# Optimization experiments

Measured on AMD Instinct MI355X. Metric: run time of the kernel, lower is better.

The kernel has to match this reference:

```python
import jax, jax.numpy as jnp
import numpy as np

B, N, E, D, H, L = 1, 50000, 800000, 128, 8, 3
HD = D // H
VOCAB = 7000
OUT = 10


def _ln(x, g, b, eps=1e-5):
    m = x.mean(-1, keepdims=True)
    v = ((x - m) ** 2).mean(-1, keepdims=True)
    return (x - m) * jax.lax.rsqrt(v + eps) * g + b


def setup_inputs() -> dict:
    key = jax.random.key(0)
    ks = jax.random.split(key, 40)
    std = 0.02 / np.sqrt(L)

    def w(k, shape):
        return (jax.random.normal(k, shape, jnp.float32) * std)

    inp = {
        "x_idx": jax.random.randint(ks[0], (B, N, 1), 0, VOCAB),
        "edge_index": jax.random.randint(ks[1], (2, E), 0, B * N),
        "emb": jax.random.normal(ks[2], (VOCAB, D), jnp.float32) * 0.02,
        # per-layer params stacked on leading L axis; linears stored [in, out]
        "Wq": w(ks[3], (L, D, D)), "bq": jnp.zeros((L, D), jnp.float32),
        "Wk": w(ks[4], (L, D, D)), "bk": jnp.zeros((L, D), jnp.float32),
        "Wv": w(ks[5], (L, D, D)), "bv": jnp.zeros((L, D), jnp.float32),
        "Wo": w(ks[6], (L, D, D)), "bo": jnp.zeros((L, D), jnp.float32),
        "g1": jnp.ones((L, D), jnp.float32), "be1": jnp.zeros((L, D), jnp.float32),
        "Wf1": w(ks[7], (L, D, 2 * D)), "bf1": jnp.zeros((L, 2 * D), jnp.float32),
        "Wf2": w(ks[8], (L, 2 * D, D)), "bf2": jnp.zeros((L, D), jnp.float32),
        "g2": jnp.ones((L, D), jnp.float32), "be2": jnp.zeros((L, D), jnp.float32),
        # MLPReadout: D -> D/2 -> D/4 -> OUT
        "mW0": w(ks[9], (D, D // 2)), "mb0": jnp.zeros((D // 2,), jnp.float32),
        "mW1": w(ks[10], (D // 2, D // 4)), "mb1": jnp.zeros((D // 4,), jnp.float32),
        "mW2": w(ks[11], (D // 4, OUT)), "mb2": jnp.zeros((OUT,), jnp.float32),
    }
    return inp


def reference(x_idx, edge_index, emb, Wq, bq, Wk, bk, Wv, bv, Wo, bo,
              g1, be1, Wf1, bf1, Wf2, bf2, g2, be2,
              mW0, mb0, mW1, mb1, mW2, mb2):
    # node embedding: sum over feature-index axis -> [B, N, D]
    x = emb[x_idx].sum(axis=-2)
    e0, e1 = edge_index[0], edge_index[1]
    scale = jnp.sqrt(jnp.float32(HD))

    for l in range(L):
        h = x
        hf = h.reshape(B * N, D)
        q = (hf @ Wq[l] + bq[l]).reshape(B * N, H, HD)
        k = (hf @ Wk[l] + bk[l]).reshape(B * N, H, HD)
        v = (hf @ Wv[l] + bv[l]).reshape(B * N, H, HD)
        # edge-indexed gather-mul-exp  [E, H, 1]
        score = jnp.clip(jnp.sum(k[e0] * q[e1], axis=-1, keepdims=True) / scale,
                         -5.0, 5.0)
        score = jnp.exp(score)
        msg = v[e0] * score                                    # [E, H, HD]
        wV = jax.ops.segment_sum(msg, e1, num_segments=B * N)  # [B*N, H, HD]
        Z = jax.ops.segment_sum(score, e1, num_segments=B * N) # [B*N, H, 1]
        attn = (wV / (Z + 1e-6)).reshape(B, N, D)
        y = attn @ Wo[l] + bo[l]
        x = _ln(h + y, g1[l], be1[l])
        # note: FFN input is y (attention output), per the original code
        y2 = jnp.maximum(y @ Wf1[l] + bf1[l], 0.0) @ Wf2[l] + bf2[l]
        x = _ln(x + y2, g2[l], be2[l])

    out = x.mean(axis=1)  # [B, D]
    out = jnp.maximum(out @ mW0 + mb0, 0.0)
    out = jnp.maximum(out @ mW1 + mb1, 0.0)
    return out @ mW2 + mb2  # [B, OUT]
```

## Files before the change

kernel.cpp:

```cpp
#include <hip/hip_runtime.h>
#include <hip/hip_bf16.h>

#define N_NODES 50000
#define N_EDGES 800000
#define DIM 128
#define NLAYERS 3

typedef short bf16x8 __attribute__((ext_vector_type(8)));
typedef float floatx4 __attribute__((ext_vector_type(4)));
typedef float floatx2 __attribute__((ext_vector_type(2)));

__device__ __forceinline__ unsigned short f2bf(float f) {
  unsigned int u = __builtin_bit_cast(unsigned int, f);
  return (unsigned short)((u + 0x7FFFu + ((u >> 16) & 1u)) >> 16);
}
__device__ __forceinline__ float bf2f(unsigned short h) {
  return __builtin_bit_cast(float, (unsigned int)h << 16);
}

__global__ __launch_bounds__(256) void embed_kernel(
    const int* __restrict__ idx, const float* __restrict__ emb,
    unsigned short* __restrict__ xb)
{
  int gid = blockIdx.x * 256 + threadIdx.x;
  int n = gid >> 5;
  int c = (gid & 31) << 2;
  if (n >= N_NODES) return;
  int e = idx[n];
  float4 val = *(const float4*)(emb + (size_t)e * DIM + c);
  ushort4 pk;
  pk.x = f2bf(val.x); pk.y = f2bf(val.y); pk.z = f2bf(val.z); pk.w = f2bf(val.w);
  *(ushort4*)(xb + (size_t)n * DIM + c) = pk;
}

__global__ __launch_bounds__(256) void hist_kernel(
    const int* __restrict__ e1, int* __restrict__ counts,
    int* __restrict__ rank)
{
  int i = blockIdx.x * 256 + threadIdx.x;
  if (i < N_EDGES) rank[i] = atomicAdd(&counts[e1[i]], 1);
}

__global__ __launch_bounds__(256) void scan_local(
    const int* __restrict__ counts, int* __restrict__ offsets,
    int* __restrict__ bsums)
{
  __shared__ int buf[256];
  int t = threadIdx.x;
  int i = blockIdx.x * 256 + t;
  int v = (i < N_NODES) ? counts[i] : 0;
  buf[t] = v;
  __syncthreads();
  int s = v;
#pragma unroll
  for (int off = 1; off < 256; off <<= 1) {
    int t2 = (t >= off) ? buf[t - off] : 0;
    __syncthreads();
    s += t2;
    buf[t] = s;
    __syncthreads();
  }
  if (i < N_NODES) offsets[i] = s - v;
  if (t == 255) bsums[blockIdx.x] = s;
}

__global__ void scan_bsums(int* __restrict__ bsums, int nblk)
{
  __shared__ int buf[256];
  int t = threadIdx.x;
  int v = (t < nblk) ? bsums[t] : 0;
  buf[t] = v;
  __syncthreads();
  int s = v;
#pragma unroll
  for (int off = 1; off < 256; off <<= 1) {
    int t2 = (t >= off) ? buf[t - off] : 0;
    __syncthreads();
    s += t2;
    buf[t] = s;
    __syncthreads();
  }
  if (t < nblk) bsums[t] = s - v;
}

__global__ __launch_bounds__(256) void scan_add(
    int* __restrict__ offsets, const int* __restrict__ bsums)
{
  int i = blockIdx.x * 256 + threadIdx.x;
  if (i < N_NODES) offsets[i] += bsums[blockIdx.x];
  if (i == 0) offsets[N_NODES] = N_EDGES;
}

__global__ __launch_bounds__(256) void scatter_kernel(
    const int* __restrict__ e0, const int* __restrict__ e1,
    const int* __restrict__ offsets, const int* __restrict__ rank,
    int* __restrict__ csr)
{
  int i = blockIdx.x * 256 + threadIdx.x;
  if (i >= N_EDGES) return;
  csr[offsets[e1[i]] + rank[i]] = e0[i];
}

__global__ __launch_bounds__(256) void prep_all(
    const float* __restrict__ Wq, const float* __restrict__ Wk,
    const float* __restrict__ Wv, const float* __restrict__ Wo,
    const float* __restrict__ Wf1, const float* __restrict__ Wf2,
    unsigned short* __restrict__ wqkv, unsigned short* __restrict__ wo,
    unsigned short* __restrict__ wf1, unsigned short* __restrict__ wf2)
{
  int g = blockIdx.x * 256 + threadIdx.x;
  if (g < 18432) {
    int srcId = g / 6144; int rem = g - srcId * 6144;
    const float* W = (srcId == 0) ? Wq : (srcId == 1) ? Wk : Wv;
    int l = rem / 2048; int r2 = rem & 2047; int kq = r2 >> 7; int n = r2 & 127;
    const float* Wl = W + (size_t)l * 128 * 128;
    unsigned short* base = wqkv + (size_t)l * 128 * 384 + (size_t)(kq * 384 + srcId * 128 + n) * 8;
#pragma unroll
    for (int j = 0; j < 8; j++)
      base[j] = f2bf(Wl[(size_t)(kq * 8 + j) * 128 + n]);
    return;
  }
  g -= 18432;
  if (g < 6144) {
    int l = g / 2048; int r2 = g & 2047; int kq = r2 >> 7; int n = r2 & 127;
    const float* Wl = Wo + (size_t)l * 128 * 128;
    unsigned short* base = wo + (size_t)l * 128 * 128 + (size_t)(kq * 128 + n) * 8;
#pragma unroll
    for (int j = 0; j < 8; j++)
      base[j] = f2bf(Wl[(size_t)(kq * 8 + j) * 128 + n]);
    return;
  }
  g -= 6144;
  if (g < 12288) {
    int l = g / 4096; int r2 = g & 4095; int kq = r2 >> 8; int n = r2 & 255;
    const float* Wl = Wf1 + (size_t)l * 128 * 256;
    unsigned short* base = wf1 + (size_t)l * 128 * 256 + (size_t)(kq * 256 + n) * 8;
#pragma unroll
    for (int j = 0; j < 8; j++)
      base[j] = f2bf(Wl[(size_t)(kq * 8 + j) * 256 + n]);
    return;
  }
  g -= 12288;
  if (g < 12288) {
    int l = g / 4096; int r2 = g & 4095; int kq = r2 >> 7; int n = r2 & 127;
    const float* Wl = Wf2 + (size_t)l * 256 * 128;
    unsigned short* base = wf2 + (size_t)l * 256 * 128 + (size_t)(kq * 128 + n) * 8;
#pragma unroll
    for (int j = 0; j < 8; j++)
      base[j] = f2bf(Wl[(size_t)(kq * 8 + j) * 128 + n]);
  }
}

#define LSTR 136

__global__ __launch_bounds__(256) void qkv0_kernel(
    const unsigned short* __restrict__ xb,
    const unsigned short* __restrict__ wqkv,
    const float* __restrict__ bq, const float* __restrict__ bk,
    const float* __restrict__ bv,
    unsigned short* __restrict__ qkv, int nrows)
{
  __shared__ unsigned short XR[64 * LSTR];
  int tid = threadIdx.x;
  int wave = tid >> 6, lane = tid & 63;
  int quad = lane >> 4, l16 = lane & 15;
  int rbase = blockIdx.x * 64;
  int wrow = wave * 16;
  int rowg = min(rbase + wrow + l16, nrows - 1);
  int lrow_v = (wrow + l16) * LSTR + quad * 8;
  bool wr = (rbase + wrow + l16 < nrows);

  bf16x8 avQ[4];
  {
    const unsigned short* arow = xb + (size_t)rowg * 128 + quad * 8;
#pragma unroll
    for (int kb = 0; kb < 4; kb++)
      avQ[kb] = *(const bf16x8*)(arow + kb * 32);
  }
#pragma unroll
  for (int c = 0; c < 3; c++) {
    floatx4 accQ[8];
#pragma unroll
    for (int ct = 0; ct < 8; ct++) accQ[ct] = (floatx4)(0.f);
#pragma unroll
    for (int kb = 0; kb < 4; kb++) {
      int kq = kb * 4 + quad;
      bf16x8 bh[8];
#pragma unroll
      for (int ct = 0; ct < 8; ct++)
        bh[ct] = *(const bf16x8*)&wqkv[(size_t)(kq * 384 + c * 128 + ct * 16 + l16) * 8];
#pragma unroll
      for (int ct = 0; ct < 8; ct++)
        accQ[ct] = __builtin_amdgcn_mfma_f32_16x16x32_bf16(avQ[kb], bh[ct], accQ[ct], 0, 0, 0);
    }
    const float* bias = (c == 0) ? bq : (c == 1) ? bk : bv;
#pragma unroll
    for (int ct = 0; ct < 8; ct++) {
      float bvv = bias[ct * 16 + l16];
#pragma unroll
      for (int i = 0; i < 4; i++)
        XR[(wrow + quad * 4 + i) * LSTR + ct * 16 + l16] = f2bf(accQ[ct][i] + bvv);
    }
    if (wr) {
      if (c == 0) {
#pragma unroll
        for (int kb = 0; kb < 4; kb++)
          *(bf16x8*)&qkv[(size_t)(rbase + wrow + l16) * 256 + kb * 32 + quad * 8] =
              *(bf16x8*)&XR[lrow_v + kb * 32];
      } else {
#pragma unroll
        for (int kb = 0; kb < 4; kb++) {
          bf16x8 w = *(bf16x8*)&XR[lrow_v + kb * 32];
          int p0 = __builtin_amdgcn_cvt_pk_fp8_f32(
              bf2f((unsigned short)w[0]) * 8.f, bf2f((unsigned short)w[1]) * 8.f, 0, false);
          int p1 = __builtin_amdgcn_cvt_pk_fp8_f32(
              bf2f((unsigned short)w[2]) * 8.f, bf2f((unsigned short)w[3]) * 8.f, 0, false);
          int p2 = __builtin_amdgcn_cvt_pk_fp8_f32(
              bf2f((unsigned short)w[4]) * 8.f, bf2f((unsigned short)w[5]) * 8.f, 0, false);
          int p3 = __builtin_amdgcn_cvt_pk_fp8_f32(
              bf2f((unsigned short)w[6]) * 8.f, bf2f((unsigned short)w[7]) * 8.f, 0, false);
          int2 st;
          st.x = (p0 & 0xffff) | (p1 << 16);
          st.y = (p2 & 0xffff) | (p3 << 16);
          *(int2*)&qkv[(size_t)(rbase + wrow + l16) * 256 + 128 + (c - 1) * 64 +
                       kb * 16 + quad * 4] = st;
        }
      }
    }
  }
}

template<bool LAST>
__global__ __launch_bounds__(256) void chainM_kernel(
    const unsigned short* __restrict__ a,
    unsigned short* __restrict__ xb,
    unsigned short* __restrict__ qkv,
    const unsigned short* __restrict__ wo, const float* __restrict__ bo,
    const float* __restrict__ g1, const float* __restrict__ be1,
    const unsigned short* __restrict__ wf1, const float* __restrict__ bf1,
    const unsigned short* __restrict__ wf2, const float* __restrict__ bf2,
    const float* __restrict__ g2, const float* __restrict__ be2,
    const unsigned short* __restrict__ wqkv,
    const float* __restrict__ bq, const float* __restrict__ bk,
    const float* __restrict__ bv, int nrows)
{
  __shared__ unsigned short Y[64 * LSTR];
  __shared__ unsigned short F[64 * LSTR];
  int tid = threadIdx.x;
  int wave = tid >> 6, lane = tid & 63;
  int quad = lane >> 4, l16 = lane & 15;
  int rbase = blockIdx.x * 64;
  int wrow = wave * 16;
  int rowg = min(rbase + wrow + l16, nrows - 1);
  int lrow_v = (wrow + l16) * LSTR + quad * 8;
  bool wr = (rbase + wrow + l16 < nrows);

#pragma unroll
  for (int kb = 0; kb < 4; kb++)
    *(bf16x8*)&F[lrow_v + kb * 32] =
        *(const bf16x8*)&xb[(size_t)rowg * 128 + kb * 32 + quad * 8];

  floatx4 accO[8];
#pragma unroll
  for (int cc = 0; cc < 8; cc++) accO[cc] = (floatx4)(0.f);
  {
    const unsigned short* arow = a + (size_t)rowg * 128 + quad * 8;
#pragma unroll
    for (int kb = 0; kb < 4; kb++) {
      bf16x8 av = *(const bf16x8*)(arow + kb * 32);
      int kq = kb * 4 + quad;
      bf16x8 bh[8];
#pragma unroll
      for (int cc = 0; cc < 8; cc++)
        bh[cc] = *(const bf16x8*)&wo[(size_t)(kq * 128 + cc * 16 + l16) * 8];
#pragma unroll
      for (int cc = 0; cc < 8; cc++)
        accO[cc] = __builtin_amdgcn_mfma_f32_16x16x32_bf16(av, bh[cc], accO[cc], 0, 0, 0);
    }
  }

  float x1v[8][4];
  {
    float biasO[8], g1v[8], b1v[8];
#pragma unroll
    for (int cc = 0; cc < 8; cc++) {
      int col = cc * 16 + l16;
      biasO[cc] = bo[col]; g1v[cc] = g1[col]; b1v[cc] = be1[col];
    }
#pragma unroll
    for (int i = 0; i < 4; i++) {
      int lrow = wrow + quad * 4 + i;
      float t[8]; float s = 0.f;
#pragma unroll
      for (int cc = 0; cc < 8; cc++) {
        float yv = accO[cc][i] + biasO[cc];
        Y[lrow * LSTR + cc * 16 + l16] = f2bf(yv);
        t[cc] = yv + bf2f(F[lrow * LSTR + cc * 16 + l16]);
        s += t[cc];
      }
      s += __shfl_xor(s, 1); s += __shfl_xor(s, 2);
      s += __shfl_xor(s, 4); s += __shfl_xor(s, 8);
      float mean = s * (1.f / 128.f);
      float vv = 0.f;
#pragma unroll
      for (int cc = 0; cc < 8; cc++) { float d = t[cc] - mean; vv += d * d; }
      vv += __shfl_xor(vv, 1); vv += __shfl_xor(vv, 2);
      vv += __shfl_xor(vv, 4); vv += __shfl_xor(vv, 8);
      float inv = rsqrtf(vv * (1.f / 128.f) + 1e-5f);
#pragma unroll
      for (int cc = 0; cc < 8; cc++)
        x1v[cc][i] = bf2f(f2bf((t[cc] - mean) * inv * g1v[cc] + b1v[cc]));
    }
  }

  bf16x8 avY[4];
#pragma unroll
  for (int kb = 0; kb < 4; kb++)
    avY[kb] = *(bf16x8*)&Y[lrow_v + kb * 32];
  floatx4 acc2[8];
#pragma unroll
  for (int cc = 0; cc < 8; cc++) acc2[cc] = (floatx4)(0.f);
#pragma unroll
  for (int h = 0; h < 2; h++) {
    floatx4 accF[8];
#pragma unroll
    for (int cc = 0; cc < 8; cc++) accF[cc] = (floatx4)(0.f);
#pragma unroll
    for (int kb = 0; kb < 4; kb++) {
      int kq = kb * 4 + quad;
      bf16x8 bh[8];
#pragma unroll
      for (int cc = 0; cc < 8; cc++)
        bh[cc] = *(const bf16x8*)&wf1[(size_t)(kq * 256 + h * 128 + cc * 16 + l16) * 8];
#pragma unroll
      for (int cc = 0; cc < 8; cc++)
        accF[cc] = __builtin_amdgcn_mfma_f32_16x16x32_bf16(avY[kb], bh[cc], accF[cc], 0, 0, 0);
    }
#pragma unroll
    for (int i = 0; i < 4; i++) {
      int lrow = wrow + quad * 4 + i;
#pragma unroll
      for (int cc = 0; cc < 8; cc++)
        F[lrow * LSTR + cc * 16 + l16] =
            f2bf(fmaxf(accF[cc][i] + bf1[h * 128 + cc * 16 + l16], 0.f));
    }
#pragma unroll
    for (int kb = 0; kb < 4; kb++) {
      bf16x8 avF = *(bf16x8*)&F[lrow_v + kb * 32];
      int kq = h * 16 + kb * 4 + quad;
      bf16x8 bh[8];
#pragma unroll
      for (int cc = 0; cc < 8; cc++)
        bh[cc] = *(const bf16x8*)&wf2[(size_t)(kq * 128 + cc * 16 + l16) * 8];
#pragma unroll
      for (int cc = 0; cc < 8; cc++)
        acc2[cc] = __builtin_amdgcn_mfma_f32_16x16x32_bf16(avF, bh[cc], acc2[cc], 0, 0, 0);
    }
  }

  {
    float bias2[8], g2v[8], b2v[8];
#pragma unroll
    for (int cc = 0; cc < 8; cc++) {
      int col = cc * 16 + l16;
      bias2[cc] = bf2[col]; g2v[cc] = g2[col]; b2v[cc] = be2[col];
    }
#pragma unroll
    for (int i = 0; i < 4; i++) {
      int lrow = wrow + quad * 4 + i;
      float t[8]; float s = 0.f;
#pragma unroll
      for (int cc = 0; cc < 8; cc++) {
        t[cc] = acc2[cc][i] + bias2[cc] + x1v[cc][i];
        s += t[cc];
      }
      s += __shfl_xor(s, 1); s += __shfl_xor(s, 2);
      s += __shfl_xor(s, 4); s += __shfl_xor(s, 8);
      float mean = s * (1.f / 128.f);
      float vv = 0.f;
#pragma unroll
      for (int cc = 0; cc < 8; cc++) { float d = t[cc] - mean; vv += d * d; }
      vv += __shfl_xor(vv, 1); vv += __shfl_xor(vv, 2);
      vv += __shfl_xor(vv, 4); vv += __shfl_xor(vv, 8);
      float inv = rsqrtf(vv * (1.f / 128.f) + 1e-5f);
#pragma unroll
      for (int cc = 0; cc < 8; cc++)
        Y[lrow * LSTR + cc * 16 + l16] =
            f2bf((t[cc] - mean) * inv * g2v[cc] + b2v[cc]);
    }
  }
  if (wr) {
#pragma unroll
    for (int kb = 0; kb < 4; kb++)
      *(bf16x8*)&xb[(size_t)(rbase + wrow + l16) * 128 + kb * 32 + quad * 8] =
          *(bf16x8*)&Y[lrow_v + kb * 32];
  }

  if (!LAST) {
    bf16x8 avQ[4];
#pragma unroll
    for (int kb = 0; kb < 4; kb++)
      avQ[kb] = *(bf16x8*)&Y[lrow_v + kb * 32];
#pragma unroll
    for (int c = 0; c < 3; c++) {
      floatx4 accQ[8];
#pragma unroll
      for (int ct = 0; ct < 8; ct++) accQ[ct] = (floatx4)(0.f);
#pragma unroll
      for (int kb = 0; kb < 4; kb++) {
        int kq = kb * 4 + quad;
        bf16x8 bh[8];
#pragma unroll
        for (int ct = 0; ct < 8; ct++)
          bh[ct] = *(const bf16x8*)&wqkv[(size_t)(kq * 384 + c * 128 + ct * 16 + l16) * 8];
#pragma unroll
        for (int ct = 0; ct < 8; ct++)
          accQ[ct] = __builtin_amdgcn_mfma_f32_16x16x32_bf16(avQ[kb], bh[ct], accQ[ct], 0, 0, 0);
      }
      const float* bias = (c == 0) ? bq : (c == 1) ? bk : bv;
#pragma unroll
      for (int ct = 0; ct < 8; ct++) {
        float bvv = bias[ct * 16 + l16];
#pragma unroll
        for (int i = 0; i < 4; i++)
          F[(wrow + quad * 4 + i) * LSTR + ct * 16 + l16] = f2bf(accQ[ct][i] + bvv);
      }
      if (wr) {
        if (c == 0) {
#pragma unroll
          for (int kb = 0; kb < 4; kb++)
            *(bf16x8*)&qkv[(size_t)(rbase + wrow + l16) * 256 + kb * 32 + quad * 8] =
                *(bf16x8*)&F[lrow_v + kb * 32];
        } else {
#pragma unroll
          for (int kb = 0; kb < 4; kb++) {
            bf16x8 w = *(bf16x8*)&F[lrow_v + kb * 32];
            int p0 = __builtin_amdgcn_cvt_pk_fp8_f32(
                bf2f((unsigned short)w[0]) * 8.f, bf2f((unsigned short)w[1]) * 8.f, 0, false);
            int p1 = __builtin_amdgcn_cvt_pk_fp8_f32(
                bf2f((unsigned short)w[2]) * 8.f, bf2f((unsigned short)w[3]) * 8.f, 0, false);
            int p2 = __builtin_amdgcn_cvt_pk_fp8_f32(
                bf2f((unsigned short)w[4]) * 8.f, bf2f((unsigned short)w[5]) * 8.f, 0, false);
            int p3 = __builtin_amdgcn_cvt_pk_fp8_f32(
                bf2f((unsigned short)w[6]) * 8.f, bf2f((unsigned short)w[7]) * 8.f, 0, false);
            int2 st;
            st.x = (p0 & 0xffff) | (p1 << 16);
            st.y = (p2 & 0xffff) | (p3 << 16);
            *(int2*)&qkv[(size_t)(rbase + wrow + l16) * 256 + 128 + (c - 1) * 64 +
                         kb * 16 + quad * 4] = st;
          }
        }
      }
    }
  }
}
#undef LSTR

#define ATTN_C8 0.04508422003f
#define ATTN_L  7.21347520444f
__device__ __forceinline__ float edge_score8(float p) {
  float t = fminf(fmaxf(p * ATTN_C8, -ATTN_L), ATTN_L);
  return __builtin_amdgcn_exp2f(t);
}
__global__ __launch_bounds__(256) void attn_kernel(
    const unsigned short* __restrict__ qkv,
    const int* __restrict__ offsets, const int* __restrict__ csr,
    unsigned short* __restrict__ attn)
{
  int node = blockIdx.x * 8 + (threadIdx.x >> 5);
  int l32 = threadIdx.x & 31;
  if (node >= N_NODES) return;
  float q0, q1, q2v, q3;
  {
    ushort4 qu = *(const ushort4*)(qkv + (size_t)node * 256 + l32 * 4);
    q0 = bf2f(qu.x); q1 = bf2f(qu.y); q2v = bf2f(qu.z); q3 = bf2f(qu.w);
  }
  const unsigned short* kb8 = qkv + 128 + l32 * 2;
  const unsigned short* vb8 = qkv + 192 + l32 * 2;
  float w0 = 0.f, w1 = 0.f, w2 = 0.f, w3 = 0.f, z = 0.f;
  int j = offsets[node], end = offsets[node + 1];
  for (; j + 4 <= end; j += 4) {
    int s[4];
#pragma unroll
    for (int u = 0; u < 4; u++) s[u] = csr[j + u] << 8;
    unsigned int ku[4], vu[4];
#pragma unroll
    for (int u = 0; u < 4; u++) {
      ku[u] = *(const unsigned int*)(kb8 + s[u]);
      vu[u] = *(const unsigned int*)(vb8 + s[u]);
    }
    float p[4];
#pragma unroll
    for (int u = 0; u < 4; u++) {
      floatx2 ka = __builtin_amdgcn_cvt_pk_f32_fp8((int)ku[u], false);
      floatx2 kc = __builtin_amdgcn_cvt_pk_f32_fp8((int)ku[u], true);
      p[u] = fmaf(ka[0], q0, fmaf(ka[1], q1, fmaf(kc[0], q2v, kc[1] * q3)));
    }
#pragma unroll
    for (int u = 0; u < 4; u++) p[u] += __shfl_xor(p[u], 1);
#pragma unroll
    for (int u = 0; u < 4; u++) p[u] += __shfl_xor(p[u], 2);
#pragma unroll
    for (int u = 0; u < 4; u++) {
      float sc = edge_score8(p[u]);
      floatx2 va = __builtin_amdgcn_cvt_pk_f32_fp8((int)vu[u], false);
      floatx2 vc = __builtin_amdgcn_cvt_pk_f32_fp8((int)vu[u], true);
      w0 = fmaf(sc, va[0], w0); w1 = fmaf(sc, va[1], w1);
      w2 = fmaf(sc, vc[0], w2); w3 = fmaf(sc, vc[1], w3);
      z += sc;
    }
  }
  for (; j < end; ++j) {
    int s = csr[j] << 8;
    unsigned int ku = *(const unsigned int*)(kb8 + s);
    unsigned int vu = *(const unsigned int*)(vb8 + s);
    floatx2 ka = __builtin_amdgcn_cvt_pk_f32_fp8((int)ku, false);
    floatx2 kc = __builtin_amdgcn_cvt_pk_f32_fp8((int)ku, true);
    float p = fmaf(ka[0], q0, fmaf(ka[1], q1, fmaf(kc[0], q2v, kc[1] * q3)));
    p += __shfl_xor(p, 1); p += __shfl_xor(p, 2);
    float sc = edge_score8(p);
    floatx2 va = __builtin_amdgcn_cvt_pk_f32_fp8((int)vu, false);
    floatx2 vc = __builtin_amdgcn_cvt_pk_f32_fp8((int)vu, true);
    w0 = fmaf(sc, va[0], w0); w1 = fmaf(sc, va[1], w1);
    w2 = fmaf(sc, vc[0], w2); w3 = fmaf(sc, vc[1], w3);
    z += sc;
  }
  float inv = 1.f / (8.f * z + 8e-6f);
  ushort4 pk;
  pk.x = f2bf(w0 * inv); pk.y = f2bf(w1 * inv);
  pk.z = f2bf(w2 * inv); pk.w = f2bf(w3 * inv);
  *(ushort4*)(attn + (size_t)node * DIM + l32 * 4) = pk;
}

#define CM_BLOCKS 128
__global__ __launch_bounds__(256) void colsum_partial(
    const unsigned short* __restrict__ xb, float* __restrict__ partial)
{
  int cg = threadIdx.x & 15;
  int ro = threadIdx.x >> 4;
  int rows = (N_NODES + CM_BLOCKS - 1) / CM_BLOCKS;
  int r0 = blockIdx.x * rows;
  int r1 = min(r0 + rows, N_NODES);
  float acc[8];
#pragma unroll
  for (int j = 0; j < 8; j++) acc[j] = 0.f;
  int r = r0 + ro;
  for (; r + 48 < r1; r += 64) {
    bf16x8 v0 = *(const bf16x8*)&xb[(size_t)r * 128 + cg * 8];
    bf16x8 v1 = *(const bf16x8*)&xb[(size_t)(r + 16) * 128 + cg * 8];
    bf16x8 v2 = *(const bf16x8*)&xb[(size_t)(r + 32) * 128 + cg * 8];
    bf16x8 v3 = *(const bf16x8*)&xb[(size_t)(r + 48) * 128 + cg * 8];
#pragma unroll
    for (int j = 0; j < 8; j++)
      acc[j] += (bf2f((unsigned short)v0[j]) + bf2f((unsigned short)v1[j])) +
                (bf2f((unsigned short)v2[j]) + bf2f((unsigned short)v3[j]));
  }
  for (; r < r1; r += 16) {
    bf16x8 v = *(const bf16x8*)&xb[(size_t)r * 128 + cg * 8];
#pragma unroll
    for (int j = 0; j < 8; j++) acc[j] += bf2f((unsigned short)v[j]);
  }
  __shared__ float s[16 * 128];
#pragma unroll
  for (int j = 0; j < 8; j++) s[ro * 128 + cg * 8 + j] = acc[j];
  __syncthreads();
#pragma unroll
  for (int step = 8; step >= 1; step >>= 1) {
    if (ro < step) {
#pragma unroll
      for (int j = 0; j < 8; j++)
        s[ro * 128 + cg * 8 + j] += s[(ro + step) * 128 + cg * 8 + j];
    }
    __syncthreads();
  }
  if (ro < 2) {
    int c = ro * 64 + cg * 4;
    *(float4*)&partial[(size_t)blockIdx.x * 128 + c] = *(float4*)&s[c];
  }
}

__global__ void readout_kernel(
    const float* __restrict__ partial,
    const float* __restrict__ mW0, const float* __restrict__ mb0,
    const float* __restrict__ mW1, const float* __restrict__ mb1,
    const float* __restrict__ mW2, const float* __restrict__ mb2,
    float* __restrict__ out)
{
  __shared__ float sx[128], h0[64], h1[32];
  int t = threadIdx.x;
  {
    float s0 = 0.f, s1 = 0.f, s2 = 0.f, s3 = 0.f;
#pragma unroll 2
    for (int p = 0; p < CM_BLOCKS; p += 4) {
      s0 += partial[(size_t)p * 128 + t];
      s1 += partial[(size_t)(p + 1) * 128 + t];
      s2 += partial[(size_t)(p + 2) * 128 + t];
      s3 += partial[(size_t)(p + 3) * 128 + t];
    }
    sx[t] = ((s0 + s1) + (s2 + s3)) * (1.f / (float)N_NODES);
  }
  __syncthreads();
  if (t < 64) {
    float a = mb0[t];
    for (int i = 0; i < 128; i++) a = fmaf(sx[i], mW0[i * 64 + t], a);
    h0[t] = fmaxf(a, 0.f);
  }
  __syncthreads();
  if (t < 32) {
    float a = mb1[t];
    for (int i = 0; i < 64; i++) a = fmaf(h0[i], mW1[i * 32 + t], a);
    h1[t] = fmaxf(a, 0.f);
  }
  __syncthreads();
  if (t < 10) {
    float a = mb2[t];
    for (int i = 0; i < 32; i++) a = fmaf(h1[i], mW2[i * 10 + t], a);
    out[t] = a;
  }
}

extern "C" void kernel_launch(void* const* d_in, const int* in_sizes, int n_in,
                              void* d_out, int out_size, void* d_ws, size_t ws_size,
                              hipStream_t stream) {
  const int*   x_idx = (const int*)d_in[0];
  const int*   eidx  = (const int*)d_in[1];
  const float* emb   = (const float*)d_in[2];
  const float* Wq = (const float*)d_in[3];  const float* bq = (const float*)d_in[4];
  const float* Wk = (const float*)d_in[5];  const float* bk = (const float*)d_in[6];
  const float* Wv = (const float*)d_in[7];  const float* bv = (const float*)d_in[8];
  const float* Wo = (const float*)d_in[9];  const float* bo = (const float*)d_in[10];
  const float* g1 = (const float*)d_in[11]; const float* be1 = (const float*)d_in[12];
  const float* Wf1 = (const float*)d_in[13]; const float* bf1 = (const float*)d_in[14];
  const float* Wf2 = (const float*)d_in[15]; const float* bf2 = (const float*)d_in[16];
  const float* g2 = (const float*)d_in[17]; const float* be2 = (const float*)d_in[18];
  const float* mW0 = (const float*)d_in[19]; const float* mb0 = (const float*)d_in[20];
  const float* mW1 = (const float*)d_in[21]; const float* mb1 = (const float*)d_in[22];
  const float* mW2 = (const float*)d_in[23]; const float* mb2 = (const float*)d_in[24];
  float* out = (float*)d_out;

  const size_t NX = (size_t)N_NODES * DIM;
  unsigned short* xb  = (unsigned short*)d_ws;
  unsigned short* qkv = xb + NX;
  unsigned short* a   = qkv + (size_t)N_NODES * 256;

  unsigned short* wqkv_p = a + NX;
  unsigned short* wo_p   = wqkv_p + 3 * 128 * 384;
  unsigned short* wf1_p  = wo_p   + 3 * 128 * 128;
  unsigned short* wf2_p  = wf1_p  + 3 * 128 * 256;
  unsigned short* wend   = wf2_p  + 3 * 256 * 128;

  int* counts    = (int*)wend;
  float* partial = (float*)(counts + N_NODES);
  int* offsets   = (int*)(partial + CM_BLOCKS * 128);
  int* bsums     = offsets + N_NODES + 1;
  int* csr       = bsums + 256;
  int* rank      = csr + N_EDGES;

  const int* e0 = eidx;
  const int* e1 = eidx + N_EDGES;

  hipMemsetAsync(counts, 0, N_NODES * sizeof(int), stream);

  prep_all<<<192, 256, 0, stream>>>(Wq, Wk, Wv, Wo, Wf1, Wf2,
                                    wqkv_p, wo_p, wf1_p, wf2_p);

  embed_kernel<<<(N_NODES * 32 + 255) / 256, 256, 0, stream>>>(x_idx, emb, xb);
  hist_kernel<<<(N_EDGES + 255) / 256, 256, 0, stream>>>(e1, counts, rank);
  int nblk = (N_NODES + 255) / 256;
  scan_local<<<nblk, 256, 0, stream>>>(counts, offsets, bsums);
  scan_bsums<<<1, 256, 0, stream>>>(bsums, nblk);
  scan_add<<<nblk, 256, 0, stream>>>(offsets, bsums);
  scatter_kernel<<<(N_EDGES + 255) / 256, 256, 0, stream>>>(e0, e1, offsets, rank, csr);

  int gc = (N_NODES + 63) / 64;
  int nb8 = (N_NODES + 7) / 8;

  qkv0_kernel<<<gc, 256, 0, stream>>>(xb, wqkv_p, bq, bk, bv, qkv, N_NODES);

  for (int l = 0; l < NLAYERS; ++l) {
    const unsigned short* wo_l   = wo_p   + (size_t)l * 128 * 128;
    const unsigned short* wf1_l  = wf1_p  + (size_t)l * 128 * 256;
    const unsigned short* wf2_l  = wf2_p  + (size_t)l * 256 * 128;
    const unsigned short* wqkv_n = wqkv_p + (size_t)(l + 1) * 128 * 384;
    const float* bo_l  = bo  + (size_t)l * DIM;
    const float* g1_l  = g1  + (size_t)l * DIM;
    const float* be1_l = be1 + (size_t)l * DIM;
    const float* bf1_l = bf1 + (size_t)l * 2 * DIM;
    const float* bf2_l = bf2 + (size_t)l * DIM;
    const float* g2_l  = g2  + (size_t)l * DIM;
    const float* be2_l = be2 + (size_t)l * DIM;

    attn_kernel<<<nb8, 256, 0, stream>>>(qkv, offsets, csr, a);
    if (l < NLAYERS - 1) {
      chainM_kernel<false><<<gc, 256, 0, stream>>>(
          a, xb, qkv, wo_l, bo_l, g1_l, be1_l, wf1_l, bf1_l, wf2_l, bf2_l,
          g2_l, be2_l, wqkv_n,
          bq + (size_t)(l + 1) * DIM, bk + (size_t)(l + 1) * DIM,
          bv + (size_t)(l + 1) * DIM, N_NODES);
    } else {
      chainM_kernel<true><<<gc, 256, 0, stream>>>(
          a, xb, qkv, wo_l, bo_l, g1_l, be1_l, wf1_l, bf1_l, wf2_l, bf2_l,
          g2_l, be2_l, wqkv_p, bq, bk, bv, N_NODES);
    }
  }

  colsum_partial<<<CM_BLOCKS, 256, 0, stream>>>(xb, partial);
  readout_kernel<<<1, 128, 0, stream>>>(partial, mW0, mb0, mW1, mb1, mW2, mb2, out);
}
```

Measured before the change: 442.9 us.

## Fuse edge attention aggregation into the per-layer chain kernel with ping-pong QKV buffers

The separate attention kernel is folded into the start of the chain kernel. Each block now aggregates edges for its own 64 nodes, with two nodes per wave at a time, and writes the normalized attention rows straight into shared memory. This removes one launch per layer and the global round trip of the attention tensor. Because other blocks still read QKV for neighbour gathers, QKV is double-buffered between layers, and the residual x is now read from global memory instead of being staged in shared memory. The catch is lower parallelism for the irregular gather phase: 782 blocks each process 8 serial node iterations, so latency hiding may be worse than with the standalone kernel.

```diff
diff --git a/kernel.cpp b/kernel.cpp
--- a/kernel.cpp
+++ b/kernel.cpp
@@ -230,11 +230,18 @@
   }
 }
 
+#define ATTN_C8 0.04508422003f
+#define ATTN_L  7.21347520444f
+__device__ __forceinline__ float edge_score8(float p) {
+  float t = fminf(fmaxf(p * ATTN_C8, -ATTN_L), ATTN_L);
+  return __builtin_amdgcn_exp2f(t);
+}
 template<bool LAST>
-__global__ __launch_bounds__(256) void chainM_kernel(
-    const unsigned short* __restrict__ a,
+__global__ __launch_bounds__(256) void chainA_kernel(
+    const unsigned short* __restrict__ qkv_in,
+    const int* __restrict__ offsets, const int* __restrict__ csr,
     unsigned short* __restrict__ xb,
-    unsigned short* __restrict__ qkv,
+    unsigned short* __restrict__ qkv_out,
     const unsigned short* __restrict__ wo, const float* __restrict__ bo,
     const float* __restrict__ g1, const float* __restrict__ be1,
     const unsigned short* __restrict__ wf1, const float* __restrict__ bf1,
@@ -249,34 +256,100 @@
   int tid = threadIdx.x;
   int wave = tid >> 6, lane = tid & 63;
   int quad = lane >> 4, l16 = lane & 15;
+  int half = lane >> 5, l32 = lane & 31;
   int rbase = blockIdx.x * 64;
   int wrow = wave * 16;
   int rowg = min(rbase + wrow + l16, nrows - 1);
   int lrow_v = (wrow + l16) * LSTR + quad * 8;
   bool wr = (rbase + wrow + l16 < nrows);
 
+  {
+    const unsigned short* kb8 = qkv_in + 128 + l32 * 2;
+    const unsigned short* vb8 = qkv_in + 192 + l32 * 2;
+#pragma unroll 1
+    for (int p = 0; p < 8; p++) {
+      int nodeL = wrow + p * 2 + half;
+      int node = rbase + nodeL;
+      if (node >= nrows) node = nrows - 1;
+      float q0, q1, q2v, q3;
+      {
+        ushort4 qu = *(const ushort4*)(qkv_in + (size_t)node * 256 + l32 * 4);
+        q0 = bf2f(qu.x); q1 = bf2f(qu.y); q2v = bf2f(qu.z); q3 = bf2f(qu.w);
+      }
+      float w0 = 0.f, w1 = 0.f, w2 = 0.f, w3 = 0.f, z = 0.f;
+      int j = offsets[node], end = offsets[node + 1];
+      for (; j + 4 <= end; j += 4) {
+        int s[4];
+#pragma unroll
+        for (int u = 0; u < 4; u++) s[u] = csr[j + u] << 8;
+        unsigned int ku[4], vu[4];
+#pragma unroll
+        for (int u = 0; u < 4; u++) {
+          ku[u] = *(const unsigned int*)(kb8 + s[u]);
+          vu[u] = *(const unsigned int*)(vb8 + s[u]);
+        }
+        float pp[4];
+#pragma unroll
+        for (int u = 0; u < 4; u++) {
+          floatx2 ka = __builtin_amdgcn_cvt_pk_f32_fp8((int)ku[u], false);
+          floatx2 kc = __builtin_amdgcn_cvt_pk_f32_fp8((int)ku[u], true);
+          pp[u] = fmaf(ka[0], q0, fmaf(ka[1], q1, fmaf(kc[0], q2v, kc[1] * q3)));
+        }
+#pragma unroll
+        for (int u = 0; u < 4; u++) pp[u] += __shfl_xor(pp[u], 1);
+#pragma unroll
+        for (int u = 0; u < 4; u++) pp[u] += __shfl_xor(pp[u], 2);
+#pragma unroll
+        for (int u = 0; u < 4; u++) {
+          float sc = edge_score8(pp[u]);
+          floatx2 va = __builtin_amdgcn_cvt_pk_f32_fp8((int)vu[u], false);
+          floatx2 vc = __builtin_amdgcn_cvt_pk_f32_fp8((int)vu[u], true);
+          w0 = fmaf(sc, va[0], w0); w1 = fmaf(sc, va[1], w1);
+          w2 = fmaf(sc, vc[0], w2); w3 = fmaf(sc, vc[1], w3);
+          z += sc;
+        }
+      }
+      for (; j < end; ++j) {
+        int s = csr[j] << 8;
+        unsigned int ku = *(const unsigned int*)(kb8 + s);
+        unsigned int vu = *(const unsigned int*)(vb8 + s);
+        floatx2 ka = __builtin_amdgcn_cvt_pk_f32_fp8((int)ku, false);
+        floatx2 kc = __builtin_amdgcn_cvt_pk_f32_fp8((int)ku, true);
+        float pv = fmaf(ka[0], q0, fmaf(ka[1], q1, fmaf(kc[0], q2v, kc[1] * q3)));
+        pv += __shfl_xor(pv, 1); pv += __shfl_xor(pv, 2);
+        float sc = edge_score8(pv);
+        floatx2 va = __builtin_amdgcn_cvt_pk_f32_fp8((int)vu, false);
+        floatx2 vc = __builtin_amdgcn_cvt_pk_f32_fp8((int)vu, true);
+        w0 = fmaf(sc, va[0], w0); w1 = fmaf(sc, va[1], w1);
+        w2 = fmaf(sc, vc[0], w2); w3 = fmaf(sc, vc[1], w3);
+        z += sc;
+      }
+      float inv = 1.f / (8.f * z + 8e-6f);
+      ushort4 pk;
+      pk.x = f2bf(w0 * inv); pk.y = f2bf(w1 * inv);
+      pk.z = f2bf(w2 * inv); pk.w = f2bf(w3 * inv);
+      *(ushort4*)&F[nodeL * LSTR + l32 * 4] = pk;
+    }
+  }
+
+  bf16x8 avO[4];
 #pragma unroll
   for (int kb = 0; kb < 4; kb++)
-    *(bf16x8*)&F[lrow_v + kb * 32] =
-        *(const bf16x8*)&xb[(size_t)rowg * 128 + kb * 32 + quad * 8];
+    avO[kb] = *(bf16x8*)&F[lrow_v + kb * 32];
 
   floatx4 accO[8];
 #pragma unroll
   for (int cc = 0; cc < 8; cc++) accO[cc] = (floatx4)(0.f);
-  {
-    const unsigned short* arow = a + (size_t)rowg * 128 + quad * 8;
-#pragma unroll
-    for (int kb = 0; kb < 4; kb++) {
-      bf16x8 av = *(const bf16x8*)(arow + kb * 32);
-      int kq = kb * 4 + quad;
-      bf16x8 bh[8];
-#pragma unroll
-      for (int cc = 0; cc < 8; cc++)
-        bh[cc] = *(const bf16x8*)&wo[(size_t)(kq * 128 + cc * 16 + l16) * 8];
-#pragma unroll
-      for (int cc = 0; cc < 8; cc++)
-        accO[cc] = __builtin_amdgcn_mfma_f32_16x16x32_bf16(av, bh[cc], accO[cc], 0, 0, 0);
-    }
+#pragma unroll
+  for (int kb = 0; kb < 4; kb++) {
+    int kq = kb * 4 + quad;
+    bf16x8 bh[8];
+#pragma unroll
+    for (int cc = 0; cc < 8; cc++)
+      bh[cc] = *(const bf16x8*)&wo[(size_t)(kq * 128 + cc * 16 + l16) * 8];
+#pragma unroll
+    for (int cc = 0; cc < 8; cc++)
+      accO[cc] = __builtin_amdgcn_mfma_f32_16x16x32_bf16(avO[kb], bh[cc], accO[cc], 0, 0, 0);
   }
 
   float x1v[8][4];
@@ -290,12 +363,13 @@
 #pragma unroll
     for (int i = 0; i < 4; i++) {
       int lrow = wrow + quad * 4 + i;
+      int growc = min(rbase + lrow, nrows - 1);
       float t[8]; float s = 0.f;
 #pragma unroll
       for (int cc = 0; cc < 8; cc++) {
         float yv = accO[cc][i] + biasO[cc];
         Y[lrow * LSTR + cc * 16 + l16] = f2bf(yv);
-        t[cc] = yv + bf2f(F[lrow * LSTR + cc * 16 + l16]);
+        t[cc] = yv + bf2f(xb[(size_t)growc * 128 + cc * 16 + l16]);
         s += t[cc];
       }
       s += __shfl_xor(s, 1); s += __shfl_xor(s, 2);
@@ -429,7 +503,7 @@
         if (c == 0) {
 #pragma unroll
           for (int kb = 0; kb < 4; kb++)
-            *(bf16x8*)&qkv[(size_t)(rbase + wrow + l16) * 256 + kb * 32 + quad * 8] =
+            *(bf16x8*)&qkv_out[(size_t)(rbase + wrow + l16) * 256 + kb * 32 + quad * 8] =
                 *(bf16x8*)&F[lrow_v + kb * 32];
         } else {
 #pragma unroll
@@ -446,8 +520,8 @@
             int2 st;
             st.x = (p0 & 0xffff) | (p1 << 16);
             st.y = (p2 & 0xffff) | (p3 << 16);
-            *(int2*)&qkv[(size_t)(rbase + wrow + l16) * 256 + 128 + (c - 1) * 64 +
-                         kb * 16 + quad * 4] = st;
+            *(int2*)&qkv_out[(size_t)(rbase + wrow + l16) * 256 + 128 + (c - 1) * 64 +
+                             kb * 16 + quad * 4] = st;
           }
         }
       }
@@ -455,82 +529,6 @@
   }
 }
 #undef LSTR
-
-#define ATTN_C8 0.04508422003f
-#define ATTN_L  7.21347520444f
-__device__ __forceinline__ float edge_score8(float p) {
-  float t = fminf(fmaxf(p * ATTN_C8, -ATTN_L), ATTN_L);
-  return __builtin_amdgcn_exp2f(t);
-}
-__global__ __launch_bounds__(256) void attn_kernel(
-    const unsigned short* __restrict__ qkv,
-    const int* __restrict__ offsets, const int* __restrict__ csr,
-    unsigned short* __restrict__ attn)
-{
-  int node = blockIdx.x * 8 + (threadIdx.x >> 5);
-  int l32 = threadIdx.x & 31;
-  if (node >= N_NODES) return;
-  float q0, q1, q2v, q3;
-  {
-    ushort4 qu = *(const ushort4*)(qkv + (size_t)node * 256 + l32 * 4);
-    q0 = bf2f(qu.x); q1 = bf2f(qu.y); q2v = bf2f(qu.z); q3 = bf2f(qu.w);
-  }
-  const unsigned short* kb8 = qkv + 128 + l32 * 2;
-  const unsigned short* vb8 = qkv + 192 + l32 * 2;
-  float w0 = 0.f, w1 = 0.f, w2 = 0.f, w3 = 0.f, z = 0.f;
-  int j = offsets[node], end = offsets[node + 1];
-  for (; j + 4 <= end; j += 4) {
-    int s[4];
-#pragma unroll
-    for (int u = 0; u < 4; u++) s[u] = csr[j + u] << 8;
-    unsigned int ku[4], vu[4];
-#pragma unroll
-    for (int u = 0; u < 4; u++) {
-      ku[u] = *(const unsigned int*)(kb8 + s[u]);
-      vu[u] = *(const unsigned int*)(vb8 + s[u]);
-    }
-    float p[4];
-#pragma unroll
-    for (int u = 0; u < 4; u++) {
-      floatx2 ka = __builtin_amdgcn_cvt_pk_f32_fp8((int)ku[u], false);
-      floatx2 kc = __builtin_amdgcn_cvt_pk_f32_fp8((int)ku[u], true);
-      p[u] = fmaf(ka[0], q0, fmaf(ka[1], q1, fmaf(kc[0], q2v, kc[1] * q3)));
-    }
-#pragma unroll
-    for (int u = 0; u < 4; u++) p[u] += __shfl_xor(p[u], 1);
-#pragma unroll
-    for (int u = 0; u < 4; u++) p[u] += __shfl_xor(p[u], 2);
-#pragma unroll
-    for (int u = 0; u < 4; u++) {
-      float sc = edge_score8(p[u]);
-      floatx2 va = __builtin_amdgcn_cvt_pk_f32_fp8((int)vu[u], false);
-      floatx2 vc = __builtin_amdgcn_cvt_pk_f32_fp8((int)vu[u], true);
-      w0 = fmaf(sc, va[0], w0); w1 = fmaf(sc, va[1], w1);
-      w2 = fmaf(sc, vc[0], w2); w3 = fmaf(sc, vc[1], w3);
-      z += sc;
-    }
-  }
-  for (; j < end; ++j) {
-    int s = csr[j] << 8;
-    unsigned int ku = *(const unsigned int*)(kb8 + s);
-    unsigned int vu = *(const unsigned int*)(vb8 + s);
-    floatx2 ka = __builtin_amdgcn_cvt_pk_f32_fp8((int)ku, false);
-    floatx2 kc = __builtin_amdgcn_cvt_pk_f32_fp8((int)ku, true);
-    float p = fmaf(ka[0], q0, fmaf(ka[1], q1, fmaf(kc[0], q2v, kc[1] * q3)));
-    p += __shfl_xor(p, 1); p += __shfl_xor(p, 2);
-    float sc = edge_score8(p);
-    floatx2 va = __builtin_amdgcn_cvt_pk_f32_fp8((int)vu, false);
-    floatx2 vc = __builtin_amdgcn_cvt_pk_f32_fp8((int)vu, true);
-    w0 = fmaf(sc, va[0], w0); w1 = fmaf(sc, va[1], w1);
-    w2 = fmaf(sc, vc[0], w2); w3 = fmaf(sc, vc[1], w3);
-    z += sc;
-  }
-  float inv = 1.f / (8.f * z + 8e-6f);
-  ushort4 pk;
-  pk.x = f2bf(w0 * inv); pk.y = f2bf(w1 * inv);
-  pk.z = f2bf(w2 * inv); pk.w = f2bf(w3 * inv);
-  *(ushort4*)(attn + (size_t)node * DIM + l32 * 4) = pk;
-}
 
 #define CM_BLOCKS 128
 __global__ __launch_bounds__(256) void colsum_partial(
@@ -639,11 +637,11 @@
   float* out = (float*)d_out;
 
   const size_t NX = (size_t)N_NODES * DIM;
-  unsigned short* xb  = (unsigned short*)d_ws;
-  unsigned short* qkv = xb + NX;
-  unsigned short* a   = qkv + (size_t)N_NODES * 256;
-
-  unsigned short* wqkv_p = a + NX;
+  unsigned short* xb   = (unsigned short*)d_ws;
+  unsigned short* qkvA = xb + NX;
+  unsigned short* qkvB = qkvA + (size_t)N_NODES * 256;
+
+  unsigned short* wqkv_p = qkvB + (size_t)N_NODES * 256;
   unsigned short* wo_p   = wqkv_p + 3 * 128 * 384;
   unsigned short* wf1_p  = wo_p   + 3 * 128 * 128;
   unsigned short* wf2_p  = wf1_p  + 3 * 128 * 256;
@@ -673,9 +671,8 @@
   scatter_kernel<<<(N_EDGES + 255) / 256, 256, 0, stream>>>(e0, e1, offsets, rank, csr);
 
   int gc = (N_NODES + 63) / 64;
-  int nb8 = (N_NODES + 7) / 8;
-
-  qkv0_kernel<<<gc, 256, 0, stream>>>(xb, wqkv_p, bq, bk, bv, qkv, N_NODES);
+
+  qkv0_kernel<<<gc, 256, 0, stream>>>(xb, wqkv_p, bq, bk, bv, qkvA, N_NODES);
 
   for (int l = 0; l < NLAYERS; ++l) {
     const unsigned short* wo_l   = wo_p   + (size_t)l * 128 * 128;
@@ -689,18 +686,20 @@
     const float* bf2_l = bf2 + (size_t)l * DIM;
     const float* g2_l  = g2  + (size_t)l * DIM;
     const float* be2_l = be2 + (size_t)l * DIM;
-
-    attn_kernel<<<nb8, 256, 0, stream>>>(qkv, offsets, csr, a);
+    unsigned short* qin  = (l & 1) ? qkvB : qkvA;
+    unsigned short* qout = (l & 1) ? qkvA : qkvB;
+
     if (l < NLAYERS - 1) {
-      chainM_kernel<false><<<gc, 256, 0, stream>>>(
-          a, xb, qkv, wo_l, bo_l, g1_l, be1_l, wf1_l, bf1_l, wf2_l, bf2_l,
-          g2_l, be2_l, wqkv_n,
+      chainA_kernel<false><<<gc, 256, 0, stream>>>(
+          qin, offsets, csr, xb, qout, wo_l, bo_l, g1_l, be1_l,
+          wf1_l, bf1_l, wf2_l, bf2_l, g2_l, be2_l, wqkv_n,
           bq + (size_t)(l + 1) * DIM, bk + (size_t)(l + 1) * DIM,
           bv + (size_t)(l + 1) * DIM, N_NODES);
     } else {
-      chainM_kernel<true><<<gc, 256, 0, stream>>>(
-          a, xb, qkv, wo_l, bo_l, g1_l, be1_l, wf1_l, bf1_l, wf2_l, bf2_l,
-          g2_l, be2_l, wqkv_p, bq, bk, bv, N_NODES);
+      chainA_kernel<true><<<gc, 256, 0, stream>>>(
+          qin, offsets, csr, xb, qout, wo_l, bo_l, g1_l, be1_l,
+          wf1_l, bf1_l, wf2_l, bf2_l, g2_l, be2_l, wqkv_p,
+          bq, bk, bv, N_NODES);
     }
   }
 
```

Measured after the change: 724.9 us. +63.7%, slower.
